# Kernel tuning notes

Hardware: AMD Instinct MI355X
Metric: run time of the kernel (lower is better)

Reference implementation:

```python
import jax, jax.numpy as jnp
import numpy as np

B, F, D = 4096, 39, 128          # batch, num_fields, embed_dim
FIELD_DIM = 10000                # per-field vocab (uniform)
K_SPACE = [1, 256, 512]
M_SPACE = [1, 2, 4]
THRESHOLD = 500
NUM = F                          # prior_flag all ones -> num == field_len
# pairs (j, m) actually used by forward: (0,0) plus all (j>=1, m)
PAIRS = [(0, 0)] + [(j, m) for j in range(1, len(K_SPACE)) for m in range(len(M_SPACE))]

def _rows(j, m):
    return NUM * THRESHOLD if j == 0 else NUM * K_SPACE[j]

def setup_inputs() -> dict:
    key = jax.random.key(0)
    ks = jax.random.split(key, 2 + 2 * len(PAIRS))
    inp = {
        "x": jax.random.randint(ks[0], (B, F), 0, FIELD_DIM),
        "arch_prob": jax.random.uniform(ks[1], (F, len(K_SPACE) * len(M_SPACE)), dtype=jnp.float32),
    }
    for n, (j, m) in enumerate(PAIRS):
        rows = _rows(j, m)
        inp[f"cb_{j}_{m}"] = jax.random.normal(ks[2 + 2 * n], (rows, D), dtype=jnp.float32)
        inp[f"idx_{j}_{m}"] = jax.random.randint(ks[3 + 2 * n], (F * FIELD_DIM, M_SPACE[m]), 0, rows)
    return inp

def reference(x, arch_prob, cb_0_0, idx_0_0, cb_1_0, idx_1_0, cb_1_1, idx_1_1,
              cb_1_2, idx_1_2, cb_2_0, idx_2_0, cb_2_1, idx_2_1, cb_2_2, idx_2_2):
    cbs = {(0, 0): cb_0_0, (1, 0): cb_1_0, (1, 1): cb_1_1, (1, 2): cb_1_2,
           (2, 0): cb_2_0, (2, 1): cb_2_1, (2, 2): cb_2_2}
    idxs = {(0, 0): idx_0_0, (1, 0): idx_1_0, (1, 1): idx_1_1, (1, 2): idx_1_2,
            (2, 0): idx_2_0, (2, 1): idx_2_1, (2, 2): idx_2_2}
    offsets = (FIELD_DIM * jnp.arange(F)).astype(x.dtype)   # offsets_a
    xg = x + offsets[None, :]                               # (B, F) global feature ids
    nM = len(M_SPACE)
    emb = jnp.zeros((B, F, D), dtype=jnp.float32)
    for (j, m) in PAIRS:                                    # small fixed set of 7 codebooks
        Mn = M_SPACE[m]
        plen = D // Mn
        idx = idxs[(j, m)][xg]                              # (B, F, Mn) codeword ids
        # original gathers the full row then slices [i*plen:(i+1)*plen] for subvector i;
        # reshape the codebook to (rows, Mn, plen) and gather only the needed slice.
        cb = cbs[(j, m)].reshape(-1, Mn, plen)
        gathered = cb[idx, jnp.arange(Mn)[None, None, :], :]  # (B, F, Mn, plen)
        scale = arch_prob[:, j * nM + m]                    # (F,) per-field arch weight
        emb = emb + (scale[None, :, None, None] * gathered).reshape(B, F, D)
    return emb
```

## Files before the change

kernel.cpp:

```cpp
#include <hip/hip_runtime.h>

#define BB 4096
#define FF 39
#define DD 128
#define FIELD_DIM 10000
#define NITEMS (BB * FF)
#define ROWS_WS_BYTES ((size_t)4 * NITEMS * 16)

__global__ __launch_bounds__(256) void pass1_resolve(
    const int* __restrict__ x,
    const int* __restrict__ i00, const int* __restrict__ i10,
    const int* __restrict__ i11, const int* __restrict__ i12,
    const int* __restrict__ i20, const int* __restrict__ i21,
    const int* __restrict__ i22,
    uint4* __restrict__ rows_ws)
{
    const int nwg = gridDim.x;
    const int cpx = nwg >> 3;
    const int blk = blockIdx.x;
    const int wg  = (blk & 7) * cpx + (blk >> 3);
    const int i   = wg * 256 + (int)threadIdx.x;
    const int f   = i >> 12;
    const int b   = i & (BB - 1);
    const int xg  = x[b * FF + f] + f * FIELD_DIM;

    const unsigned r00 = (unsigned)i00[xg];
    const unsigned r10 = (unsigned)i10[xg];
    const unsigned r20 = (unsigned)i20[xg];
    const int2 v11 = *reinterpret_cast<const int2*>(i11 + (size_t)xg * 2);
    const int2 v21 = *reinterpret_cast<const int2*>(i21 + (size_t)xg * 2);
    const int4 v12 = *reinterpret_cast<const int4*>(i12 + (size_t)xg * 4);
    const int4 v22 = *reinterpret_cast<const int4*>(i22 + (size_t)xg * 4);

    const unsigned w0 = r00 | (r10 << 16);
    const unsigned r11k[2] = { (unsigned)v11.x, (unsigned)v11.y };
    const unsigned r21k[2] = { (unsigned)v21.x, (unsigned)v21.y };
    const unsigned r12k[4] = { (unsigned)v12.x, (unsigned)v12.y,
                               (unsigned)v12.z, (unsigned)v12.w };
    const unsigned r22k[4] = { (unsigned)v22.x, (unsigned)v22.y,
                               (unsigned)v22.z, (unsigned)v22.w };

#pragma unroll
    for (int q = 0; q < 4; ++q) {
        uint4 rec;
        rec.x = w0;
        rec.y = r20 | (r11k[q >> 1] << 16);
        rec.z = r21k[q >> 1] | (r12k[q] << 16);
        rec.w = r22k[q];
        rows_ws[(size_t)q * NITEMS + i] = rec;
    }
}

__global__ __launch_bounds__(256) void pass2_gather(
    const float* __restrict__ arch_prob,
    const float* __restrict__ cb00, const float* __restrict__ cb10,
    const float* __restrict__ cb11, const float* __restrict__ cb12,
    const float* __restrict__ cb20, const float* __restrict__ cb21,
    const float* __restrict__ cb22,
    const uint4* __restrict__ rows_ws,
    float* __restrict__ out)
{
    const int blk = blockIdx.x;
    const int xcd = blk & 7;
    const int q   = xcd >> 1;
    const int ph  = xcd & 1;
    const int seq = blk >> 3;

    const int t   = (int)threadIdx.x;
    const int li  = t & 7;
    const int ii  = ph * (NITEMS / 2) + seq * 32 + (t >> 3);
    const int f   = ii >> 12;
    const int b   = ii & (BB - 1);
    const int d0  = q * 32 + li * 4;

    const uint4 rw = rows_ws[(size_t)q * NITEMS + ii];
    const int r00 = (int)(rw.x & 0xffffu), r10 = (int)(rw.x >> 16);
    const int r20 = (int)(rw.y & 0xffffu), r11 = (int)(rw.y >> 16);
    const int r21 = (int)(rw.z & 0xffffu), r12 = (int)(rw.z >> 16);
    const int r22 = (int)(rw.w & 0xffffu);

    const float* ap = arch_prob + f * 9;

    float4 acc = make_float4(0.f, 0.f, 0.f, 0.f);

#define GATHER_FMA(cb, r, col)                                                \
    do {                                                                      \
        float4 v = *reinterpret_cast<const float4*>((cb) + (size_t)(r) * DD + d0); \
        float s = ap[col];                                                    \
        acc.x += s * v.x; acc.y += s * v.y;                                   \
        acc.z += s * v.z; acc.w += s * v.w;                                   \
    } while (0)

    GATHER_FMA(cb00, r00, 0);
    GATHER_FMA(cb10, r10, 3);
    GATHER_FMA(cb11, r11, 4);
    GATHER_FMA(cb12, r12, 5);
    GATHER_FMA(cb20, r20, 6);
    GATHER_FMA(cb21, r21, 7);
    GATHER_FMA(cb22, r22, 8);
#undef GATHER_FMA

    float* dst = out + ((size_t)b * FF + f) * DD + d0;
    __builtin_nontemporal_store(acc.x, dst + 0);
    __builtin_nontemporal_store(acc.y, dst + 1);
    __builtin_nontemporal_store(acc.z, dst + 2);
    __builtin_nontemporal_store(acc.w, dst + 3);
}

__global__ __launch_bounds__(256) void mixq_embed(
    const int* __restrict__ x,
    const float* __restrict__ arch_prob,
    const float* __restrict__ cb00, const int* __restrict__ i00,
    const float* __restrict__ cb10, const int* __restrict__ i10,
    const float* __restrict__ cb11, const int* __restrict__ i11,
    const float* __restrict__ cb12, const int* __restrict__ i12,
    const float* __restrict__ cb20, const int* __restrict__ i20,
    const float* __restrict__ cb21, const int* __restrict__ i21,
    const float* __restrict__ cb22, const int* __restrict__ i22,
    float* __restrict__ out)
{
    const int nwg  = gridDim.x;
    const int perx = nwg >> 3;
    const int blk  = blockIdx.x;
    const int xcd  = blk & 7;
    const int hh   = xcd >> 2;
    const int wh   = (xcd & 3) * perx + (blk >> 3);

    const int t   = (int)threadIdx.x;
    const int sub = (t >> 4) & 1;
    const int li  = t & 15;
    const int ii  = wh * 16 + ((t >> 5) << 1) + sub;
    const int f   = ii >> 12;
    const int bb  = ii & (BB - 1);
    const int d0  = (hh << 6) + (li << 2);

    const int xg = x[bb * FF + f] + f * FIELD_DIM;
    const float* ap = arch_prob + f * 9;
    const int k4 = (hh << 1) + (li >> 3);

    int r00 = i00[xg];
    int r10 = i10[xg];
    int r11 = i11[(size_t)xg * 2 + hh];
    int r12 = i12[(size_t)xg * 4 + k4];
    int r20 = i20[xg];
    int r21 = i21[(size_t)xg * 2 + hh];
    int r22 = i22[(size_t)xg * 4 + k4];

    float4 acc = make_float4(0.f, 0.f, 0.f, 0.f);

#define GATHER_FMA(cb, r, col)                                                \
    do {                                                                      \
        float4 v = *reinterpret_cast<const float4*>((cb) + (size_t)(r) * DD + d0); \
        float s = ap[col];                                                    \
        acc.x += s * v.x; acc.y += s * v.y;                                   \
        acc.z += s * v.z; acc.w += s * v.w;                                   \
    } while (0)

    GATHER_FMA(cb00, r00, 0);
    GATHER_FMA(cb10, r10, 3);
    GATHER_FMA(cb11, r11, 4);
    GATHER_FMA(cb12, r12, 5);
    GATHER_FMA(cb20, r20, 6);
    GATHER_FMA(cb21, r21, 7);
    GATHER_FMA(cb22, r22, 8);
#undef GATHER_FMA

    float* dst = out + ((size_t)bb * FF + f) * DD + d0;
    __builtin_nontemporal_store(acc.x, dst + 0);
    __builtin_nontemporal_store(acc.y, dst + 1);
    __builtin_nontemporal_store(acc.z, dst + 2);
    __builtin_nontemporal_store(acc.w, dst + 3);
}

extern "C" void kernel_launch(void* const* d_in, const int* in_sizes, int n_in,
                              void* d_out, int out_size, void* d_ws, size_t ws_size,
                              hipStream_t stream) {
    const int*   x  = (const int*)d_in[0];
    const float* ap = (const float*)d_in[1];
    const float* cb00 = (const float*)d_in[2];
    const int*   i00  = (const int*)d_in[3];
    const float* cb10 = (const float*)d_in[4];
    const int*   i10  = (const int*)d_in[5];
    const float* cb11 = (const float*)d_in[6];
    const int*   i11  = (const int*)d_in[7];
    const float* cb12 = (const float*)d_in[8];
    const int*   i12  = (const int*)d_in[9];
    const float* cb20 = (const float*)d_in[10];
    const int*   i20  = (const int*)d_in[11];
    const float* cb21 = (const float*)d_in[12];
    const int*   i21  = (const int*)d_in[13];
    const float* cb22 = (const float*)d_in[14];
    const int*   i22  = (const int*)d_in[15];
    float* out = (float*)d_out;

    if (ws_size >= ROWS_WS_BYTES) {
        uint4* rows_ws = (uint4*)d_ws;
        pass1_resolve<<<NITEMS / 256, 256, 0, stream>>>(
            x, i00, i10, i11, i12, i20, i21, i22, rows_ws);
        pass2_gather<<<(NITEMS / 32) * 4, 256, 0, stream>>>(
            ap, cb00, cb10, cb11, cb12, cb20, cb21, cb22, rows_ws, out);
    } else {
        const long long total_threads = (long long)BB * FF * 32;
        const int blocks = (int)((total_threads + 255) / 256);
        mixq_embed<<<blocks, 256, 0, stream>>>(
            x, ap, cb00, i00, cb10, i10, cb11, i11, cb12, i12,
            cb20, i20, cb21, i21, cb22, i22, out);
    }
}
```

Baseline: 80.16 us.

## Process four items per thread in gather pass with codebook-phased barriers

```diff
diff --git a/kernel.cpp b/kernel.cpp
--- a/kernel.cpp
+++ b/kernel.cpp
@@ -6,6 +6,8 @@
 #define FIELD_DIM 10000
 #define NITEMS (BB * FF)
 #define ROWS_WS_BYTES ((size_t)4 * NITEMS * 16)
+
+typedef unsigned uint4v __attribute__((ext_vector_type(4)));
 
 __global__ __launch_bounds__(256) void pass1_resolve(
     const int* __restrict__ x,
@@ -66,45 +68,60 @@
     const int ph  = xcd & 1;
     const int seq = blk >> 3;
 
-    const int t   = (int)threadIdx.x;
-    const int li  = t & 7;
-    const int ii  = ph * (NITEMS / 2) + seq * 32 + (t >> 3);
-    const int f   = ii >> 12;
-    const int b   = ii & (BB - 1);
-    const int d0  = q * 32 + li * 4;
-
-    const uint4 rw = rows_ws[(size_t)q * NITEMS + ii];
-    const int r00 = (int)(rw.x & 0xffffu), r10 = (int)(rw.x >> 16);
-    const int r20 = (int)(rw.y & 0xffffu), r11 = (int)(rw.y >> 16);
-    const int r21 = (int)(rw.z & 0xffffu), r12 = (int)(rw.z >> 16);
-    const int r22 = (int)(rw.w & 0xffffu);
-
-    const float* ap = arch_prob + f * 9;
-
-    float4 acc = make_float4(0.f, 0.f, 0.f, 0.f);
-
-#define GATHER_FMA(cb, r, col)                                                \
+    const int t    = (int)threadIdx.x;
+    const int li   = t & 7;
+    const int slot = t >> 3;
+    const int d0   = q * 32 + li * 4;
+    const int base = ph * (NITEMS / 2) + seq * 128 + slot;
+
+    int  ii[4];
+    int  ff[4];
+    int  bb[4];
+    uint4v rw[4];
+#pragma unroll
+    for (int j = 0; j < 4; ++j) {
+        ii[j] = base + 32 * j;
+        ff[j] = ii[j] >> 12;
+        bb[j] = ii[j] & (BB - 1);
+        rw[j] = __builtin_nontemporal_load(
+            reinterpret_cast<const uint4v*>(rows_ws + (size_t)q * NITEMS + ii[j]));
+    }
+
+    float4 acc[4];
+#pragma unroll
+    for (int j = 0; j < 4; ++j) acc[j] = make_float4(0.f, 0.f, 0.f, 0.f);
+
+#define BOOK_PHASE(cb, widx, shift, col)                                      \
     do {                                                                      \
-        float4 v = *reinterpret_cast<const float4*>((cb) + (size_t)(r) * DD + d0); \
-        float s = ap[col];                                                    \
-        acc.x += s * v.x; acc.y += s * v.y;                                   \
-        acc.z += s * v.z; acc.w += s * v.w;                                   \
+        _Pragma("unroll")                                                     \
+        for (int j = 0; j < 4; ++j) {                                         \
+            int r = (int)((rw[j][widx] >> (shift)) & 0xffffu);                \
+            float4 v = *reinterpret_cast<const float4*>(                      \
+                (cb) + (size_t)r * DD + d0);                                  \
+            float s = arch_prob[ff[j] * 9 + (col)];                           \
+            acc[j].x += s * v.x; acc[j].y += s * v.y;                         \
+            acc[j].z += s * v.z; acc[j].w += s * v.w;                         \
+        }                                                                     \
+        __syncthreads();                                                      \
     } while (0)
 
-    GATHER_FMA(cb00, r00, 0);
-    GATHER_FMA(cb10, r10, 3);
-    GATHER_FMA(cb11, r11, 4);
-    GATHER_FMA(cb12, r12, 5);
-    GATHER_FMA(cb20, r20, 6);
-    GATHER_FMA(cb21, r21, 7);
-    GATHER_FMA(cb22, r22, 8);
-#undef GATHER_FMA
-
-    float* dst = out + ((size_t)b * FF + f) * DD + d0;
-    __builtin_nontemporal_store(acc.x, dst + 0);
-    __builtin_nontemporal_store(acc.y, dst + 1);
-    __builtin_nontemporal_store(acc.z, dst + 2);
-    __builtin_nontemporal_store(acc.w, dst + 3);
+    BOOK_PHASE(cb00, 0,  0, 0);
+    BOOK_PHASE(cb10, 0, 16, 3);
+    BOOK_PHASE(cb11, 1, 16, 4);
+    BOOK_PHASE(cb12, 2, 16, 5);
+    BOOK_PHASE(cb20, 1,  0, 6);
+    BOOK_PHASE(cb21, 2,  0, 7);
+    BOOK_PHASE(cb22, 3,  0, 8);
+#undef BOOK_PHASE
+
+#pragma unroll
+    for (int j = 0; j < 4; ++j) {
+        float* dst = out + ((size_t)bb[j] * FF + ff[j]) * DD + d0;
+        __builtin_nontemporal_store(acc[j].x, dst + 0);
+        __builtin_nontemporal_store(acc[j].y, dst + 1);
+        __builtin_nontemporal_store(acc[j].z, dst + 2);
+        __builtin_nontemporal_store(acc[j].w, dst + 3);
+    }
 }
 
 __global__ __launch_bounds__(256) void mixq_embed(
@@ -197,7 +214,7 @@
         uint4* rows_ws = (uint4*)d_ws;
         pass1_resolve<<<NITEMS / 256, 256, 0, stream>>>(
             x, i00, i10, i11, i12, i20, i21, i22, rows_ws);
-        pass2_gather<<<(NITEMS / 32) * 4, 256, 0, stream>>>(
+        pass2_gather<<<(NITEMS / 128) * 4, 256, 0, stream>>>(
             ap, cb00, cb10, cb11, cb12, cb20, cb21, cb22, rows_ws, out);
     } else {
         const long long total_threads = (long long)BB * FF * 32;
```

New measurement: 77.05 us. -3.9%, faster.
